# Optimization experiments

Hardware: AMD Instinct MI355X
Metric: run time of the kernel (lower is better)

Reference implementation:

```python
import jax, jax.numpy as jnp
import numpy as np

B, T, KD, QD, AD, VD, W = 16, 4096, 1024, 1024, 512, 1024, 8


def moving_sum(x, back, forward):
    # x: [B, T] -> windowed sum over [t-back, t+forward], matches F.conv1d with ones filter
    xp = jnp.pad(x, ((0, 0), (back, forward)))[:, None, :]
    filt = jnp.ones((1, 1, back + forward + 1), x.dtype)
    y = jax.lax.conv_general_dilated(xp, filt, (1,), 'VALID')
    return y[:, 0, :]


def setup_inputs() -> dict:
    key = jax.random.key(0)
    ks = jax.random.split(key, 16)
    inp = {
        'key': jax.random.normal(ks[0], (B, T, KD), jnp.float32),
        'value': jax.random.normal(ks[1], (B, T, VD), jnp.float32),
        'query': jax.random.normal(ks[2], (B, 1, QD), jnp.float32),
        'noise': jax.random.normal(ks[3], (B, T), jnp.float32),
        'Wk_mono': jax.random.normal(ks[4], (KD, AD), jnp.float32) * (KD ** -0.5),
        'b_mono': jnp.zeros((AD,), jnp.float32),
        'Wq_mono': jax.random.normal(ks[5], (QD, AD), jnp.float32) * (QD ** -0.5),
        'Wk_chunk': jax.random.normal(ks[6], (KD, AD), jnp.float32) * (KD ** -0.5),
        'b_chunk': jnp.zeros((AD,), jnp.float32),
        'Wq_chunk': jax.random.normal(ks[7], (QD, AD), jnp.float32) * (QD ** -0.5),
        'r_mono': jnp.array([-4.0], jnp.float32),
        'r_chunk': jnp.array([-4.0], jnp.float32),
    }
    # weight-normalized v vectors: g = sqrt(1/attn_dim), w = g * v/||v||
    g = (1.0 / AD) ** 0.5
    vm = jax.random.normal(ks[8], (AD,), jnp.float32)
    vc = jax.random.normal(ks[9], (AD,), jnp.float32)
    inp['v_mono'] = g * vm / jnp.linalg.norm(vm)
    inp['v_chunk'] = g * vc / jnp.linalg.norm(vc)
    return inp


def _forward(key, value, query, noise, Wk_mono, b_mono, Wq_mono, v_mono, r_mono,
             Wk_chunk, b_chunk, Wq_chunk, v_chunk, r_chunk):
    bs, kmax = key.shape[0], key.shape[1]
    # aw_prev default: one-hot at position 0
    aw_prev = jnp.zeros((bs, kmax), key.dtype).at[:, 0].set(1.0)

    # monotonic energy: [B, T]
    qm = jnp.einsum('bqd,da->bqa', query, Wq_mono)  # [B,1,A], broadcasts over T
    e_mono = jnp.einsum('bta,a->bt', jnp.tanh(key @ Wk_mono + b_mono + qm), v_mono) + r_mono

    # parallel mode: sigmoid with additive gaussian noise
    p_choose = jax.nn.sigmoid(e_mono + noise)
    # safe_cumprod with the original's exclusive_cumsum (prepends ONES, drops last)
    log1mp = jnp.log(jnp.clip(1.0 - p_choose, 1e-10, 1.0))
    shifted = jnp.concatenate([jnp.ones((bs, 1), key.dtype), log1mp[:, :-1]], axis=1)
    cumprod_1mp = jnp.exp(jnp.cumsum(shifted, axis=1))
    aw = p_choose * cumprod_1mp * jnp.cumsum(
        aw_prev / jnp.clip(cumprod_1mp, 1e-10, 1.0), axis=1)

    # chunk energy
    qc = jnp.einsum('bqd,da->bqa', query, Wq_chunk)
    e_chunk = jnp.einsum('bta,a->bt', jnp.tanh(key @ Wk_chunk + b_chunk + qc), v_chunk) + r_chunk

    # efficient chunkwise attention
    u = e_chunk - jnp.max(e_chunk, axis=1, keepdims=True)
    softmax_exp = jnp.maximum(jnp.exp(u), 1e-5)
    denom = moving_sum(softmax_exp, back=W - 1, forward=0)
    beta = softmax_exp * moving_sum(aw / denom, back=0, forward=W - 1)

    cv = jnp.einsum('bt,btd->bd', beta, value)[:, None, :]  # [B,1,VD]
    return cv, aw[..., None]


def reference(key, value, query, noise, Wk_mono, b_mono, Wq_mono, v_mono, r_mono,
              Wk_chunk, b_chunk, Wq_chunk, v_chunk, r_chunk):
    return _forward(key, value, query, noise, Wk_mono, b_mono, Wq_mono, v_mono, r_mono,
                    Wk_chunk, b_chunk, Wq_chunk, v_chunk, r_chunk)
```

## Files before the change

### kernel.cpp

```cpp
#include <hip/hip_runtime.h>
#include <hip/hip_bf16.h>
#include <math.h>

#define B_   16
#define T_   4096
#define KD_  1024
#define AD_  512
#define VD_  1024

typedef float f32x4 __attribute__((ext_vector_type(4)));
typedef short s16x8 __attribute__((ext_vector_type(8)));

static __device__ __forceinline__ short f2bf(float f) {
    __hip_bfloat16 h = __float2bfloat16(f);
    return __builtin_bit_cast(short, h);
}

static __device__ __forceinline__ float fast_tanh(float x) {
    x = fminf(fmaxf(x, -15.f), 15.f);
    float e = __expf(2.f * x);
    return (e - 1.f) / (e + 1.f);
}

static __device__ __forceinline__ void gload16(const void* g, void* l) {
    __builtin_amdgcn_global_load_lds(
        (const __attribute__((address_space(1))) void*)(g),
        (__attribute__((address_space(3))) void*)(l), 16, 0, 0);
}


__global__ __launch_bounds__(256) void cvt_key_blk_kernel(
    const float* __restrict__ key, short* __restrict__ keyB) {
    const size_t nchunk = (size_t)B_ * T_ * KD_ / 8;
    size_t stride = (size_t)gridDim.x * 256;
    for (size_t g = (size_t)blockIdx.x * 256 + threadIdx.x; g < nchunk; g += stride) {
        const float* p = key + g * 8;
        f32x4 f0 = *reinterpret_cast<const f32x4*>(p);
        f32x4 f1 = *reinterpret_cast<const f32x4*>(p + 4);
        s16x8 h;
        h[0] = f2bf(f0[0]); h[1] = f2bf(f0[1]); h[2] = f2bf(f0[2]); h[3] = f2bf(f0[3]);
        h[4] = f2bf(f1[0]); h[5] = f2bf(f1[1]); h[6] = f2bf(f1[2]); h[7] = f2bf(f1[3]);
        size_t m = g >> 7;
        int kc = (int)(g & 127);
        size_t mt = m >> 8;
        int r = (int)(m & 255);
        int kt = kc >> 2;
        int sub = kc & 3;
        int c = (r << 2) | (sub ^ ((r >> 1) & 3));
        *reinterpret_cast<s16x8*>(keyB + (((mt * 32 + kt) * 1024 + c) << 3)) = h;
    }
}

__global__ __launch_bounds__(256) void qproj_kernel(
    const float* __restrict__ query,
    const float* __restrict__ Wq_mono, const float* __restrict__ b_mono,
    const float* __restrict__ Wq_chunk, const float* __restrict__ b_chunk,
    float* __restrict__ qb) {
    __shared__ float red[4][64];
    int b = blockIdx.x;
    int mat = blockIdx.y;
    int ac = blockIdx.z;
    const float* Wq = mat ? Wq_chunk : Wq_mono;
    const float* bb = mat ? b_chunk : b_mono;
    int al = threadIdx.x & 63;
    int dg = threadIdx.x >> 6;
    int a = ac * 64 + al;
    const float* q = query + b * KD_ + dg * 256;
    const float* wp = Wq + (size_t)(dg * 256) * AD_ + a;
    float s = 0.f;
#pragma unroll 4
    for (int d = 0; d < 256; ++d)
        s += q[d] * wp[(size_t)d * AD_];
    red[dg][al] = s;
    __syncthreads();
    if (dg == 0) {
        float t = red[0][al] + red[1][al] + red[2][al] + red[3][al];
        qb[(mat * B_ + b) * AD_ + a] = t + bb[a];
    }
}

__global__ __launch_bounds__(256) void wtrans_kernel(
    const float* __restrict__ Wk_mono, const float* __restrict__ Wk_chunk,
    short* __restrict__ WkTB) {
    __shared__ float tile[32][33];
    int n0 = blockIdx.x * 32;
    int k0 = blockIdx.y * 32;
    int tx = threadIdx.x;
    int ty = threadIdx.y;
    int tid = ty * 32 + tx;
    const float* src;
    int nloc;
    if (n0 < 512) { src = Wk_mono;  nloc = n0; }
    else          { src = Wk_chunk; nloc = n0 - 512; }
#pragma unroll
    for (int i = 0; i < 4; ++i) {
        int k = ty + i * 8;
        tile[k][tx] = src[(size_t)(k0 + k) * AD_ + nloc + tx];
    }
    __syncthreads();
    if (tid < 128) {
        int r = tid >> 2;
        int sub = tid & 3;
        s16x8 h;
#pragma unroll
        for (int j = 0; j < 8; ++j)
            h[j] = f2bf(tile[sub * 8 + j][r]);
        int n = n0 + r;
        int nblk = n >> 7;
        int rloc = n & 127;
        int kt = k0 >> 5;
        int c = (rloc << 2) | (sub ^ ((rloc >> 1) & 3));
        *reinterpret_cast<s16x8*>(WkTB + (((size_t)(nblk * 32 + kt) * 512 + c) << 3)) = h;
    }
}

__global__ __launch_bounds__(512) void gemm_e_kernel(
    const short* __restrict__ keyB,
    const short* __restrict__ WkTB,
    const float* __restrict__ qb,
    const float* __restrict__ v_mono, const float* __restrict__ v_chunk,
    float* __restrict__ e_ws ) {
    __shared__ short As[2][256 * 32];
    __shared__ short Bs[2][128 * 32];
    int tid = threadIdx.x;
    int bid = blockIdx.x;
    int swz = (bid & 7) * 256 + (bid >> 3);
    int mt = swz >> 3;
    int nt = swz & 7;
    int mBase = mt * 256;
    int nBase = nt * 128;
    int lane = tid & 63;
    int wid = tid >> 6;
    int wr = wid >> 1, wc = wid & 1;
    int col16 = lane & 15, g4 = lane >> 4;

    int cA0 = wid * 64 + lane;
    int cA1 = cA0 + 512;
    int cB  = wid * 64 + lane;
    const short* pA0 = keyB + ((size_t)mt * 32 * 1024 + cA0) * 8;
    const short* pA1 = keyB + ((size_t)mt * 32 * 1024 + cA1) * 8;
    const short* pB  = WkTB + ((size_t)nt * 32 * 512 + cB) * 8;
    int sA0 = (wid * 64) * 8;
    int sA1 = (512 + wid * 64) * 8;
    int sB  = (wid * 64) * 8;

    int aoff[4], boff[4];
#pragma unroll
    for (int m = 0; m < 4; ++m) {
        int row = wr * 64 + m * 16 + col16;
        aoff[m] = (row * 4 + (g4 ^ ((row >> 1) & 3))) * 8;
    }
#pragma unroll
    for (int n = 0; n < 4; ++n) {
        int row = wc * 64 + n * 16 + col16;
        boff[n] = (row * 4 + (g4 ^ ((row >> 1) & 3))) * 8;
    }

    f32x4 zero4 = {0.f, 0.f, 0.f, 0.f};
    f32x4 acc[4][4];
#pragma unroll
    for (int m = 0; m < 4; ++m)
#pragma unroll
        for (int n = 0; n < 4; ++n) acc[m][n] = zero4;

    gload16(pA0, &As[0][sA0]);
    gload16(pA1, &As[0][sA1]);
    gload16(pB,  &Bs[0][sB]);
    pA0 += 8192; pA1 += 8192; pB += 4096;
    __syncthreads();

    int cur = 0;
    for (int kt = 0; kt < 31; ++kt) {
        int nxt = cur ^ 1;
        gload16(pA0, &As[nxt][sA0]);
        gload16(pA1, &As[nxt][sA1]);
        gload16(pB,  &Bs[nxt][sB]);
        pA0 += 8192; pA1 += 8192; pB += 4096;
        s16x8 af[4], bfr[4];
#pragma unroll
        for (int m = 0; m < 4; ++m)
            af[m] = *reinterpret_cast<const s16x8*>(&As[cur][aoff[m]]);
#pragma unroll
        for (int n = 0; n < 4; ++n)
            bfr[n] = *reinterpret_cast<const s16x8*>(&Bs[cur][boff[n]]);
#pragma unroll
        for (int m = 0; m < 4; ++m)
#pragma unroll
            for (int n = 0; n < 4; ++n)
                acc[m][n] = __builtin_amdgcn_mfma_f32_16x16x32_bf16(af[m], bfr[n], acc[m][n], 0, 0, 0);
        __syncthreads();
        cur = nxt;
    }
    {
        s16x8 af[4], bfr[4];
#pragma unroll
        for (int m = 0; m < 4; ++m)
            af[m] = *reinterpret_cast<const s16x8*>(&As[cur][aoff[m]]);
#pragma unroll
        for (int n = 0; n < 4; ++n)
            bfr[n] = *reinterpret_cast<const s16x8*>(&Bs[cur][boff[n]]);
#pragma unroll
        for (int m = 0; m < 4; ++m)
#pragma unroll
            for (int n = 0; n < 4; ++n)
                acc[m][n] = __builtin_amdgcn_mfma_f32_16x16x32_bf16(af[m], bfr[n], acc[m][n], 0, 0, 0);
    }

    int bIdx = mBase >> 12;
    int matrix = nBase >> 9;
    int aBase = (nBase & 511) + wc * 64 + col16;
    const float* qbRow = qb + (matrix * B_ + bIdx) * AD_;
    const float* vv = matrix ? v_chunk : v_mono;
    float* eArr = e_ws + matrix * (B_ * T_);
    float qcol[4], vcol[4];
#pragma unroll
    for (int n = 0; n < 4; ++n) {
        int a = aBase + n * 16;
        qcol[n] = qbRow[a];
        vcol[n] = vv[a];
    }
#pragma unroll
    for (int m = 0; m < 4; ++m) {
        float s0 = 0.f, s1 = 0.f, s2 = 0.f, s3 = 0.f;
#pragma unroll
        for (int n = 0; n < 4; ++n) {
            s0 += fast_tanh(acc[m][n][0] + qcol[n]) * vcol[n];
            s1 += fast_tanh(acc[m][n][1] + qcol[n]) * vcol[n];
            s2 += fast_tanh(acc[m][n][2] + qcol[n]) * vcol[n];
            s3 += fast_tanh(acc[m][n][3] + qcol[n]) * vcol[n];
        }
#pragma unroll
        for (int mask = 1; mask < 16; mask <<= 1) {
            s0 += __shfl_xor(s0, mask, 64);
            s1 += __shfl_xor(s1, mask, 64);
            s2 += __shfl_xor(s2, mask, 64);
            s3 += __shfl_xor(s3, mask, 64);
        }
        if (col16 == 0) {
            int rowB = mBase + wr * 64 + m * 16 + g4 * 4;
            atomicAdd(&eArr[rowB + 0], s0);
            atomicAdd(&eArr[rowB + 1], s1);
            atomicAdd(&eArr[rowB + 2], s2);
            atomicAdd(&eArr[rowB + 3], s3);
        }
    }
}

__global__ __launch_bounds__(256) void scan_kernel(
    const float* __restrict__ e_ws,
    const float* __restrict__ noise,
    const float* __restrict__ r_mono, const float* __restrict__ r_chunk,
    float* __restrict__ aw_out, float* __restrict__ beta_out) {
    __shared__ float s_aw[T_];
    __shared__ float s_sexp[T_];
    __shared__ float s_ad[T_];
    __shared__ float s_w[4];
    int b = blockIdx.x;
    int tid = threadIdx.x;
    int lane = tid & 63;
    int wid4 = tid >> 6;
    int t0 = tid * 16;
    const float* em = e_ws + b * T_;
    const float* ec = e_ws + B_ * T_ + b * T_;
    const float* nz = noise + b * T_;
    float rm = r_mono[0], rc = r_chunk[0];

    float pv[16], lp[16];
    float run = 0.f;
#pragma unroll
    for (int j = 0; j < 16; ++j) {
        float x = em[t0 + j] + rm + nz[t0 + j];
        float p = 1.f / (1.f + expf(-x));
        pv[j] = p;
        float om = fminf(fmaxf(1.f - p, 1e-10f), 1.f);
        lp[j] = run;
        run += logf(om);
    }
    float x = run;
#pragma unroll
    for (int off = 1; off < 64; off <<= 1) {
        float y = __shfl_up(x, off, 64);
        if (lane >= off) x += y;
    }
    if (lane == 63) s_w[wid4] = x;
    __syncthreads();
    float wbase = 0.f;
#pragma unroll
    for (int i = 0; i < 3; ++i) if (i < wid4) wbase += s_w[i];
    float base = 1.f + (wbase + x - run);
#pragma unroll
    for (int j = 0; j < 16; ++j) {
        float aw = pv[j] * expf(base + lp[j]);
        s_aw[t0 + j] = aw;
        aw_out[b * T_ + t0 + j] = aw;
    }
    float evs[16];
    float lmax = -INFINITY;
#pragma unroll
    for (int j = 0; j < 16; ++j) {
        float v = ec[t0 + j] + rc;
        evs[j] = v;
        lmax = fmaxf(lmax, v);
    }
#pragma unroll
    for (int off = 1; off < 64; off <<= 1)
        lmax = fmaxf(lmax, __shfl_xor(lmax, off, 64));
    __syncthreads();
    if (lane == 0) s_w[wid4] = lmax;
    __syncthreads();
    float mx = fmaxf(fmaxf(s_w[0], s_w[1]), fmaxf(s_w[2], s_w[3]));
#pragma unroll
    for (int j = 0; j < 16; ++j)
        s_sexp[t0 + j] = fmaxf(expf(evs[j] - mx), 1e-5f);
    __syncthreads();
#pragma unroll
    for (int j = 0; j < 16; ++j) {
        int t = t0 + j;
        int lo = t - 7; if (lo < 0) lo = 0;
        float d = 0.f;
        for (int i = lo; i <= t; ++i) d += s_sexp[i];
        s_ad[t] = s_aw[t] / d;
    }
    __syncthreads();
#pragma unroll
    for (int j = 0; j < 16; ++j) {
        int t = t0 + j;
        int hi = t + 7; if (hi > T_ - 1) hi = T_ - 1;
        float m2 = 0.f;
        for (int i = t; i <= hi; ++i) m2 += s_ad[i];
        beta_out[b * T_ + t] = s_sexp[t] * m2;
    }
}

__global__ __launch_bounds__(256) void cv_kernel(
    const float* __restrict__ value,
    const float* __restrict__ beta,
    float* __restrict__ cv) {
    __shared__ float s_beta[128];
    int b = blockIdx.x;
    int tc = blockIdx.y;
    int tid = threadIdx.x;
    int t0 = tc * 128;
    if (tid < 128) s_beta[tid] = beta[b * T_ + t0 + tid];
    __syncthreads();
    int d0 = tid * 4;
    f32x4 acc = {0.f, 0.f, 0.f, 0.f};
    const float* vp = value + (size_t)(b * T_ + t0) * VD_ + d0;
#pragma unroll 4
    for (int i = 0; i < 128; ++i) {
        f32x4 v = *reinterpret_cast<const f32x4*>(vp + (size_t)i * VD_);
        float bt = s_beta[i];
        acc[0] += bt * v[0];
        acc[1] += bt * v[1];
        acc[2] += bt * v[2];
        acc[3] += bt * v[3];
    }
    atomicAdd(&cv[b * VD_ + d0 + 0], acc[0]);
    atomicAdd(&cv[b * VD_ + d0 + 1], acc[1]);
    atomicAdd(&cv[b * VD_ + d0 + 2], acc[2]);
    atomicAdd(&cv[b * VD_ + d0 + 3], acc[3]);
}

extern "C" void kernel_launch(void* const* d_in, const int* in_sizes, int n_in,
                              void* d_out, int out_size, void* d_ws, size_t ws_size,
                              hipStream_t stream) {
    const float* key      = (const float*)d_in[0];
    const float* value    = (const float*)d_in[1];
    const float* query    = (const float*)d_in[2];
    const float* noise    = (const float*)d_in[3];
    const float* Wk_mono  = (const float*)d_in[4];
    const float* b_mono   = (const float*)d_in[5];
    const float* Wq_mono  = (const float*)d_in[6];
    const float* Wk_chunk = (const float*)d_in[7];
    const float* b_chunk  = (const float*)d_in[8];
    const float* Wq_chunk = (const float*)d_in[9];
    const float* r_mono   = (const float*)d_in[10];
    const float* r_chunk  = (const float*)d_in[11];
    const float* v_mono   = (const float*)d_in[12];
    const float* v_chunk  = (const float*)d_in[13];
    float* out = (float*)d_out;

    char* ws = (char*)d_ws;
    size_t off = 0;
    float* e_ws = (float*)(ws + off); off += 2 * B_ * T_ * sizeof(float);
    float* qb   = (float*)(ws + off); off += 2 * B_ * AD_ * sizeof(float);
    short* WkTB = (short*)(ws + off); off += (size_t)KD_ * KD_ * 2;
    float* beta = (float*)(ws + off); off += B_ * T_ * sizeof(float);
    short* keyB = (short*)(ws + off);

    hipMemsetAsync(e_ws, 0, 2 * B_ * T_ * sizeof(float), stream);
    hipMemsetAsync(out, 0, B_ * VD_ * sizeof(float), stream);

    qproj_kernel<<<dim3(16, 2, 8), 256, 0, stream>>>(query, Wq_mono, b_mono, Wq_chunk, b_chunk, qb);
    wtrans_kernel<<<dim3(32, 32), dim3(32, 8), 0, stream>>>(Wk_mono, Wk_chunk, WkTB);
    cvt_key_blk_kernel<<<4096, 256, 0, stream>>>(key, keyB);
    gemm_e_kernel<<<2048, 512, 0, stream>>>(keyB, WkTB, qb, v_mono, v_chunk, e_ws);
    scan_kernel<<<16, 256, 0, stream>>>(e_ws, noise, r_mono, r_chunk, out + B_ * VD_, beta);
    cv_kernel<<<dim3(16, 32), 256, 0, stream>>>(value, beta, out);
}
```

Baseline: 370.4 us.

## Triple-buffer GEMM shared-memory stages with one barrier per k-step

Moves the energy GEMM from double to triple buffering of the A and B tiles in shared memory. Loads are issued two k-steps ahead, and each iteration waits with a partial vmcnt and a single barrier, replacing the trailing __syncthreads. The aim is to hide global-to-LDS latency better and drop one barrier per iteration. The cost is 50% more LDS per block, which can lower occupancy, and the hand-written vmcnt counts depend on how many memory instructions gload16 emits.

```diff
diff --git a/kernel.cpp b/kernel.cpp
--- a/kernel.cpp
+++ b/kernel.cpp
@@ -120,8 +120,8 @@
     const float* __restrict__ qb,
     const float* __restrict__ v_mono, const float* __restrict__ v_chunk,
     float* __restrict__ e_ws ) {
-    __shared__ short As[2][256 * 32];
-    __shared__ short Bs[2][128 * 32];
+    __shared__ short As[3][256 * 32];
+    __shared__ short Bs[3][128 * 32];
     int tid = threadIdx.x;
     int bid = blockIdx.x;
     int swz = (bid & 7) * 256 + (bid >> 3);
@@ -137,12 +137,19 @@
     int cA0 = wid * 64 + lane;
     int cA1 = cA0 + 512;
     int cB  = wid * 64 + lane;
-    const short* pA0 = keyB + ((size_t)mt * 32 * 1024 + cA0) * 8;
-    const short* pA1 = keyB + ((size_t)mt * 32 * 1024 + cA1) * 8;
-    const short* pB  = WkTB + ((size_t)nt * 32 * 512 + cB) * 8;
     int sA0 = (wid * 64) * 8;
     int sA1 = (512 + wid * 64) * 8;
     int sB  = (wid * 64) * 8;
+    const short* aTile = keyB + (size_t)mt * 32 * 1024 * 8;
+    const short* bTile = WkTB + (size_t)nt * 32 * 512 * 8;
+
+    auto stage = [&](int buf, int kt) {
+        const short* a = aTile + (size_t)kt * 1024 * 8;
+        const short* b = bTile + (size_t)kt * 512 * 8;
+        gload16(a + cA0 * 8, &As[buf][sA0]);
+        gload16(a + cA1 * 8, &As[buf][sA1]);
+        gload16(b + cB  * 8, &Bs[buf][sB]);
+    };
 
     int aoff[4], boff[4];
 #pragma unroll
@@ -163,19 +170,18 @@
 #pragma unroll
         for (int n = 0; n < 4; ++n) acc[m][n] = zero4;
 
-    gload16(pA0, &As[0][sA0]);
-    gload16(pA1, &As[0][sA1]);
-    gload16(pB,  &Bs[0][sB]);
-    pA0 += 8192; pA1 += 8192; pB += 4096;
-    __syncthreads();
+    stage(0, 0);
+    stage(1, 1);
 
     int cur = 0;
     for (int kt = 0; kt < 31; ++kt) {
-        int nxt = cur ^ 1;
-        gload16(pA0, &As[nxt][sA0]);
-        gload16(pA1, &As[nxt][sA1]);
-        gload16(pB,  &Bs[nxt][sB]);
-        pA0 += 8192; pA1 += 8192; pB += 4096;
+        asm volatile("s_waitcnt vmcnt(3)" ::: "memory");
+        __builtin_amdgcn_s_barrier();
+        asm volatile("" ::: "memory");
+        if (kt < 30) {
+            int pb = cur + 2; if (pb >= 3) pb -= 3;
+            stage(pb, kt + 2);
+        }
         s16x8 af[4], bfr[4];
 #pragma unroll
         for (int m = 0; m < 4; ++m)
@@ -188,10 +194,12 @@
 #pragma unroll
             for (int n = 0; n < 4; ++n)
                 acc[m][n] = __builtin_amdgcn_mfma_f32_16x16x32_bf16(af[m], bfr[n], acc[m][n], 0, 0, 0);
-        __syncthreads();
-        cur = nxt;
+        ++cur; if (cur == 3) cur = 0;
     }
     {
+        asm volatile("s_waitcnt vmcnt(0)" ::: "memory");
+        __builtin_amdgcn_s_barrier();
+        asm volatile("" ::: "memory");
         s16x8 af[4], bfr[4];
 #pragma unroll
         for (int m = 0; m < 4; ++m)
```

Measured after the change: 393.7 us. +6.3%, slower.
